# Performance work log

Measured on AMD Instinct MI355X. Metric: run time of the kernel, lower is better.

The kernel has to match this reference:

```python
import jax, jax.numpy as jnp
import numpy as np

B, N, FD = 2, 50000, 13
E = 250000
M, H = 128, 128          # message_dim, hidden_dim
EDGE_IN = 2 * FD + 8     # 34
NODE_IN = FD + 2 * M     # 269


def _mlp(x, w1, b1, w2, b2):
    return jnp.tanh(x @ w1 + b1) @ w2 + b2


def setup_inputs() -> dict:
    root = jax.random.key(0)
    k = lambda i: jax.random.fold_in(root, i)

    def lin(i, din, dout):
        w = jax.random.normal(k(i), (din, dout), jnp.float32) * np.float32(1.0 / np.sqrt(din))
        b = jax.random.normal(k(i + 100), (dout,), jnp.float32) * np.float32(0.01)
        return w, b

    ew1, eb1 = lin(1, EDGE_IN, H); ew2, eb2 = lin(2, H, M)      # mlp_edge
    ww1, wb1 = lin(3, EDGE_IN, H); ww2, wb2 = lin(4, H, 1)      # mlp_weight
    xw1, xb1 = lin(5, EDGE_IN, H); xw2, xb2 = lin(6, H, M)      # mlp_edge_world
    yw1, yb1 = lin(7, EDGE_IN, H); yw2, yb2 = lin(8, H, 1)      # mlp_weight_world
    nw1, nb1 = lin(9, NODE_IN, H); nw2, nb2 = lin(10, H, FD)    # mlp_node

    z_h = jax.random.normal(k(20), (B, N, FD), jnp.float32)
    edge_hh = jax.random.randint(k(21), (B, 2, E), 0, N, jnp.int32)
    edge_world = jax.random.randint(k(22), (B, 2, E), 0, N, jnp.int32)
    return dict(z_h=z_h, edge_hh=edge_hh, edge_world=edge_world,
                ew1=ew1, eb1=eb1, ew2=ew2, eb2=eb2,
                ww1=ww1, wb1=wb1, ww2=ww2, wb2=wb2,
                xw1=xw1, xb1=xb1, xw2=xw2, xb2=xb2,
                yw1=yw1, yb1=yb1, yw2=yw2, yb2=yb2,
                nw1=nw1, nb1=nb1, nw2=nw2, nb2=nb2)


def _edge_features(z, s, t):
    # z: (N, FD); s, t: (E,)
    pos, vel = z[:, 0:3], z[:, 3:6]
    diff = pos[s] - pos[t]                               # (E, 3)
    dist = jnp.sum(diff * diff, axis=-1, keepdims=True)  # (E, 1) squared distance
    vxc = jnp.cross(vel[s], vel[t])                      # (E, 3)
    vxn = jnp.linalg.norm(vxc, axis=-1, keepdims=True)   # (E, 1)
    return jnp.concatenate([diff, dist, vxc, vxn], axis=-1)  # (E, 8)


def reference(z_h, edge_hh, edge_world,
              ew1, eb1, ew2, eb2, ww1, wb1, ww2, wb2,
              xw1, xb1, xw2, xb2, yw1, yb1, yw2, yb2,
              nw1, nb1, nw2, nb2):
    n_nodes = z_h.shape[1]

    def per_batch(z, e_hh, e_w):
        # normal edges
        s, t = e_hh[0], e_hh[1]
        inp = jnp.concatenate([z[s], z[t], _edge_features(z, s, t)], axis=-1)  # (E, 34)
        m = _mlp(inp, ew1, eb1, ew2, eb2)                                       # (E, M)
        w = jax.nn.sigmoid(_mlp(inp, ww1, wb1, ww2, wb2))                       # (E, 1)
        agg_h = jnp.zeros((n_nodes, M), z.dtype).at[t].add(w * m)
        # world edges
        sw, tw = e_w[0], e_w[1]
        inpw = jnp.concatenate([z[sw], z[tw], _edge_features(z, sw, tw)], axis=-1)
        mw = _mlp(inpw, xw1, xb1, xw2, xb2)
        ww_ = jax.nn.sigmoid(_mlp(inpw, yw1, yb1, yw2, yb2))
        agg_w = jnp.zeros((n_nodes, M), z.dtype).at[tw].add(ww_ * mw)
        return agg_h, agg_w

    m_agg_h, m_agg_w = jax.vmap(per_batch)(z_h, edge_hh, edge_world)  # (B, N, M) each
    input_node = jnp.concatenate([z_h, m_agg_h, m_agg_w], axis=-1)    # (B, N, 269)
    delta_z_h = _mlp(input_node, nw1, nb1, nw2, nb2)                  # (B, N, 13)
    return delta_z_h
```

## Files before the change

kernel.cpp:

```cpp
#include <hip/hip_runtime.h>
#include <hip/hip_bf16.h>

#define B_   2
#define N_   50000
#define FD_  13
#define E_   250000
#define M_   128
#define H_   128

typedef __attribute__((ext_vector_type(8))) short  short8;
typedef __attribute__((ext_vector_type(8))) __bf16 bf16x8;
typedef __attribute__((ext_vector_type(4))) float  f32x4;
typedef __attribute__((ext_vector_type(8))) unsigned short ushort8;

#define MSG_BYTES  (4ull * E_ * 128 * 2)
#define HIST_BYTES (4ull * N_ * 4)
#define SORT_BYTES (4ull * E_ * 4)
#define OFF_EW1 0u
#define OFF_WW1 8192u
#define OFF_EW2 16384u
#define OFF_XW1 32768u
#define OFF_YW1 40960u
#define OFF_XW2 49152u
#define OFF_NW1 65536u
#define OFF_NW2 102400u

__device__ __forceinline__ float bf2f(unsigned short u) {
    unsigned int v = ((unsigned int)u) << 16;
    return __builtin_bit_cast(float, v);
}
__device__ __forceinline__ unsigned short f2bf(float f) {
    __bf16 h = (__bf16)f;
    return __builtin_bit_cast(unsigned short, h);
}
__device__ __forceinline__ float tanh_fast(float x) {
    float e = __expf(x + x);
    float r = __builtin_amdgcn_rcpf(e + 1.0f);
    return __builtin_fmaf(-2.0f, r, 1.0f);
}
__device__ __forceinline__ float sigmoid_fast(float x) {
    return __builtin_amdgcn_rcpf(1.0f + __expf(-x));
}
__device__ __forceinline__ f32x4 mfma16(short8 a, short8 b, f32x4 c) {
    return __builtin_amdgcn_mfma_f32_16x16x32_bf16(
        __builtin_bit_cast(bf16x8, a), __builtin_bit_cast(bf16x8, b), c, 0, 0, 0);
}

__global__ void prep_kernel(const float* __restrict__ ew1, const float* __restrict__ ww1,
                            const float* __restrict__ ew2, const float* __restrict__ xw1,
                            const float* __restrict__ yw1, const float* __restrict__ xw2,
                            const float* __restrict__ nw1, const float* __restrict__ nw2,
                            unsigned short* __restrict__ fb) {
    int m = blockIdx.y, f = blockIdx.x, l = threadIdx.x;
    const float* src; int K, Nn, KS; unsigned int off;
    switch (m) {
        case 0: src = ew1; K = 34;  Nn = 128; KS = 2; off = OFF_EW1; break;
        case 1: src = ww1; K = 34;  Nn = 128; KS = 2; off = OFF_WW1; break;
        case 2: src = ew2; K = 128; Nn = 128; KS = 4; off = OFF_EW2; break;
        case 3: src = xw1; K = 34;  Nn = 128; KS = 2; off = OFF_XW1; break;
        case 4: src = yw1; K = 34;  Nn = 128; KS = 2; off = OFF_YW1; break;
        case 5: src = xw2; K = 128; Nn = 128; KS = 4; off = OFF_XW2; break;
        case 6: src = nw1; K = 269; Nn = 128; KS = 9; off = OFF_NW1; break;
        default: src = nw2; K = 128; Nn = 13; KS = 4; off = OFF_NW2; break;
    }
    int NT = (Nn + 15) / 16;
    if (f >= KS * NT) return;
    int ks = f / NT, nt = f % NT;
    int n = nt * 16 + (l & 15);
    unsigned short* dst = fb + off + ((unsigned int)f * 64u + (unsigned int)l) * 8u;
    #pragma unroll
    for (int j = 0; j < 8; j++) {
        int k = ks * 32 + ((l >> 4) * 8) + j;
        int kk = k; bool valid = (k < K) && (n < Nn);
        if (m == 6) {
            if (k < 256)      kk = k + 13;
            else if (k < 269) kk = k - 256;
            else              valid = false;
            valid = valid && (n < Nn);
        }
        dst[j] = valid ? f2bf(src[kk * Nn + n]) : (unsigned short)0;
    }
}

__global__ void hist_kernel(const int* __restrict__ ehh, const int* __restrict__ eww,
                            int* __restrict__ hist) {
    int p = blockIdx.y, idx = blockIdx.x * 256 + threadIdx.x;
    if (idx >= E_) return;
    const int* eg = ((p >> 1) ? eww : ehh) + (size_t)(p & 1) * 2 * E_;
    atomicAdd(&hist[p * N_ + eg[E_ + idx]], 1);
}

__global__ void scan_kernel(int* __restrict__ hist) {
    __shared__ int part[1024];
    const int p = blockIdx.x, tid = threadIdx.x;
    int* h = hist + p * N_;
    const int lo = tid * 52;
    int cnt = N_ - lo; if (cnt < 0) cnt = 0; if (cnt > 52) cnt = 52;
    int v[52];
    int sum = 0;
    if (cnt == 52) {
        const int4* src = (const int4*)(h + lo);
        #pragma unroll
        for (int i = 0; i < 13; i++) {
            int4 t = src[i];
            v[4*i] = t.x; v[4*i+1] = t.y; v[4*i+2] = t.z; v[4*i+3] = t.w;
        }
        #pragma unroll
        for (int i = 0; i < 52; i++) sum += v[i];
    } else {
        for (int i = 0; i < cnt; i++) sum += h[lo + i];
    }
    part[tid] = sum;
    __syncthreads();
    for (int off = 1; off < 1024; off <<= 1) {
        int t = (tid >= off) ? part[tid - off] : 0;
        __syncthreads();
        part[tid] += t;
        __syncthreads();
    }
    int excl = (tid == 0) ? 0 : part[tid - 1];
    if (cnt == 52) {
        int4* dst = (int4*)(h + lo);
        #pragma unroll
        for (int i = 0; i < 13; i++) {
            int4 o;
            o.x = excl; excl += v[4*i];
            o.y = excl; excl += v[4*i+1];
            o.z = excl; excl += v[4*i+2];
            o.w = excl; excl += v[4*i+3];
            dst[i] = o;
        }
    } else {
        for (int i = 0; i < cnt; i++) { int t = h[lo + i]; h[lo + i] = excl; excl += t; }
    }
}

__global__ void scatter_kernel(const int* __restrict__ ehh, const int* __restrict__ eww,
                               int* __restrict__ hist, int* __restrict__ sorted) {
    int p = blockIdx.y, idx = blockIdx.x * 256 + threadIdx.x;
    if (idx >= E_) return;
    const int* eg = ((p >> 1) ? eww : ehh) + (size_t)(p & 1) * 2 * E_;
    int t = eg[E_ + idx];
    int pos = atomicAdd(&hist[p * N_ + t], 1);
    sorted[p * E_ + pos] = idx;
}

__launch_bounds__(256, 3)
__global__ void edge_kernel_msg(const float* __restrict__ z,
                                const int* __restrict__ ehh, const int* __restrict__ eww,
                                const int* __restrict__ sorted,
                                const unsigned short* __restrict__ fb,
                                unsigned short* __restrict__ msg,
                                const float* __restrict__ eb1, const float* __restrict__ wb1,
                                const float* __restrict__ ww2, const float* __restrict__ wb2,
                                const float* __restrict__ eb2,
                                const float* __restrict__ xb1, const float* __restrict__ yb1,
                                const float* __restrict__ yw2, const float* __restrict__ yb2,
                                const float* __restrict__ xb2) {
    __shared__ alignas(16) unsigned short Abuf[128][72];
    __shared__ alignas(16) unsigned short Hbuf[128][136];
    __shared__ float w_acc[128];

    const int tid  = threadIdx.x;
    const int lane = tid & 63, wv = tid >> 6, quad = lane >> 4, c = lane & 15;
    const int pass = blockIdx.y, b = pass & 1, set = pass >> 1;
    const int ebase = blockIdx.x * 128;

    const int* eg = (set ? eww : ehh) + (size_t)b * 2 * E_;
    const float* zb = z + (size_t)b * N_ * FD_;
    unsigned short* msgp = msg + (size_t)pass * E_ * 128;

    const short8* Fm1 = (const short8*)(fb + (set ? OFF_XW1 : OFF_EW1));
    const short8* Fw1 = (const short8*)(fb + (set ? OFF_YW1 : OFF_WW1));
    const short8* Fm2 = (const short8*)(fb + (set ? OFF_XW2 : OFF_EW2));
    const float* B1m = set ? xb1 : eb1;
    const float* B1w = set ? yb1 : wb1;
    const float* B2m = set ? xb2 : eb2;
    const float* Wv2 = set ? yw2 : ww2;
    const float wbias = (set ? yb2 : wb2)[0];

    const int nt0 = wv * 2;
    short8 bm[2][2], bw[2][2], b2f[2][4];
    float bias1m[2], bias1w[2], bias2m[2], w2v[2];
    #pragma unroll
    for (int i = 0; i < 2; i++) {
        int nt = nt0 + i, n = nt * 16 + c;
        #pragma unroll
        for (int ks = 0; ks < 2; ks++) { bm[i][ks] = Fm1[(ks * 8 + nt) * 64 + lane];
                                         bw[i][ks] = Fw1[(ks * 8 + nt) * 64 + lane]; }
        #pragma unroll
        for (int ks = 0; ks < 4; ks++) { b2f[i][ks] = Fm2[(ks * 8 + nt) * 64 + lane]; }
        bias1m[i] = B1m[n]; bias1w[i] = B1w[n];
        bias2m[i] = B2m[n]; w2v[i] = Wv2[n];
    }

    if (tid < 128) {
        const int e = tid;
        int sp = ebase + e; if (sp >= E_) sp = E_ - 1;
        int idx = sorted[(size_t)pass * E_ + sp];
        int s = eg[idx], t = eg[E_ + idx];
        w_acc[e] = 0.0f;
        const float* zs = zb + (size_t)s * 13;
        const float* zt = zb + (size_t)t * 13;
        float fs[13], ft[13];
        __builtin_memcpy(fs, zs, 13 * sizeof(float));
        __builtin_memcpy(ft, zt, 13 * sizeof(float));
        float d0 = fs[0] - ft[0], d1 = fs[1] - ft[1], d2 = fs[2] - ft[2];
        float dist = d0 * d0 + d1 * d1 + d2 * d2;
        float c0 = fs[4] * ft[5] - fs[5] * ft[4];
        float c1 = fs[5] * ft[3] - fs[3] * ft[5];
        float c2 = fs[3] * ft[4] - fs[4] * ft[3];
        float vxn = sqrtf(c0 * c0 + c1 * c1 + c2 * c2);
        unsigned short row[64];
        #pragma unroll
        for (int j = 0; j < 13; j++) { row[j] = f2bf(fs[j]); row[13 + j] = f2bf(ft[j]); }
        row[26] = f2bf(d0); row[27] = f2bf(d1); row[28] = f2bf(d2); row[29] = f2bf(dist);
        row[30] = f2bf(c0); row[31] = f2bf(c1); row[32] = f2bf(c2); row[33] = f2bf(vxn);
        #pragma unroll
        for (int j = 34; j < 64; j++) row[j] = 0;
        #pragma unroll
        for (int v = 0; v < 8; v++) {
            short8 sv;
            #pragma unroll
            for (int j = 0; j < 8; j++) sv[j] = (short)row[v * 8 + j];
            *((short8*)&Abuf[e][v * 8]) = sv;
        }
    }
    __syncthreads();

    #pragma unroll 1
    for (int rt = 0; rt < 8; rt++) {
        const unsigned short* ar = &Abuf[rt * 16 + c][0];
        short8 a0 = *((const short8*)(ar + quad * 8));
        short8 a1 = *((const short8*)(ar + 32 + quad * 8));
        float wpart[4] = {0.f, 0.f, 0.f, 0.f};
        #pragma unroll
        for (int i = 0; i < 2; i++) {
            f32x4 accm = {bias1m[i], bias1m[i], bias1m[i], bias1m[i]};
            f32x4 accw = {bias1w[i], bias1w[i], bias1w[i], bias1w[i]};
            accm = mfma16(a0, bm[i][0], accm);
            accm = mfma16(a1, bm[i][1], accm);
            accw = mfma16(a0, bw[i][0], accw);
            accw = mfma16(a1, bw[i][1], accw);
            int n = (nt0 + i) * 16 + c;
            #pragma unroll
            for (int r = 0; r < 4; r++) {
                Hbuf[rt * 16 + quad * 4 + r][n] = f2bf(tanh_fast(accm[r]));
                wpart[r] += tanh_fast(accw[r]) * w2v[i];
            }
        }
        #pragma unroll
        for (int r = 0; r < 4; r++) {
            float v = wpart[r];
            v += __shfl_xor(v, 1); v += __shfl_xor(v, 2);
            v += __shfl_xor(v, 4); v += __shfl_xor(v, 8);
            if (c == r) atomicAdd(&w_acc[rt * 16 + quad * 4 + r], v);
        }
    }
    __syncthreads();
    if (tid < 128) w_acc[tid] = sigmoid_fast(w_acc[tid] + wbias);
    __syncthreads();

    #pragma unroll 1
    for (int rt = 0; rt < 8; rt++) {
        const unsigned short* hr = &Hbuf[rt * 16 + c][0];
        short8 h0 = *((const short8*)(hr + quad * 8));
        short8 h1 = *((const short8*)(hr + 32 + quad * 8));
        short8 h2 = *((const short8*)(hr + 64 + quad * 8));
        short8 h3 = *((const short8*)(hr + 96 + quad * 8));
        const int elq = rt * 16 + quad * 4;
        const float g0 = w_acc[elq + 0], g1 = w_acc[elq + 1];
        const float g2 = w_acc[elq + 2], g3 = w_acc[elq + 3];
        #pragma unroll
        for (int i = 0; i < 2; i++) {
            f32x4 acc = {bias2m[i], bias2m[i], bias2m[i], bias2m[i]};
            acc = mfma16(h0, b2f[i][0], acc);
            acc = mfma16(h1, b2f[i][1], acc);
            acc = mfma16(h2, b2f[i][2], acc);
            acc = mfma16(h3, b2f[i][3], acc);
            const int n = (nt0 + i) * 16 + c;
            const float gv[4] = {g0, g1, g2, g3};
            #pragma unroll
            for (int r = 0; r < 4; r++) {
                int e = elq + r;
                if (ebase + e < E_)
                    msgp[(size_t)(ebase + e) * 128 + n] = f2bf(acc[r] * gv[r]);
            }
        }
    }
}

__launch_bounds__(256, 4)
__global__ void node_fused(const float* __restrict__ z,
                           const unsigned short* __restrict__ msg,
                           const int* __restrict__ hist,
                           const unsigned short* __restrict__ fb,
                           const float* __restrict__ nb1,
                           const float* __restrict__ nb2,
                           float* __restrict__ out) {
    __shared__ alignas(16) unsigned short Abuf[16][296];
    __shared__ alignas(16) unsigned short Hbuf[16][136];

    const int tid  = threadIdx.x;
    const int lane = tid & 63, wv = tid >> 6, quad = lane >> 4, c = lane & 15;
    const int g0 = blockIdx.x * 16;

    {
        const int nl = tid >> 4;
        const int part = tid & 15;
        const int g = g0 + nl;
        const int b = (g >= N_) ? 1 : 0;
        const int t = g - b * N_;
        #pragma unroll
        for (int s = 0; s < 2; s++) {
            const int p = s * 2 + b;
            const int end   = hist[p * N_ + t];
            const int start = (t > 0) ? hist[p * N_ + t - 1] : 0;
            float acc[8];
            #pragma unroll
            for (int k = 0; k < 8; k++) acc[k] = 0.f;
            const unsigned short* mp = msg + (size_t)p * E_ * 128 + part * 8;
            int j = start;
            for (; j + 4 <= end; j += 4) {
                ushort8 m0 = *(const ushort8*)(mp + (size_t)(j + 0) * 128);
                ushort8 m1 = *(const ushort8*)(mp + (size_t)(j + 1) * 128);
                ushort8 m2 = *(const ushort8*)(mp + (size_t)(j + 2) * 128);
                ushort8 m3 = *(const ushort8*)(mp + (size_t)(j + 3) * 128);
                #pragma unroll
                for (int k = 0; k < 8; k++)
                    acc[k] += (bf2f(m0[k]) + bf2f(m1[k])) + (bf2f(m2[k]) + bf2f(m3[k]));
            }
            for (; j < end; j++) {
                ushort8 m = *(const ushort8*)(mp + (size_t)j * 128);
                #pragma unroll
                for (int k = 0; k < 8; k++) acc[k] += bf2f(m[k]);
            }
            ushort8 u;
            #pragma unroll
            for (int k = 0; k < 8; k++) u[k] = f2bf(acc[k]);
            *((ushort8*)&Abuf[nl][s * 128 + part * 8]) = u;
        }
    }
    for (int j = tid; j < 16 * 13; j += 256) {
        int nl = j / 13, k = j % 13;
        Abuf[nl][256 + k] = f2bf(z[(size_t)(g0 + nl) * 13 + k]);
    }
    for (int j = tid; j < 16 * 19; j += 256) {
        int nl = j / 19, k = j % 19;
        Abuf[nl][269 + k] = 0;
    }
    __syncthreads();

    {
        const short8* F1 = (const short8*)(fb + OFF_NW1);
        const int nt0 = wv * 2;
        const float b1a = nb1[nt0 * 16 + c];
        const float b1b = nb1[(nt0 + 1) * 16 + c];
        f32x4 acc0 = {b1a, b1a, b1a, b1a};
        f32x4 acc1 = {b1b, b1b, b1b, b1b};
        #pragma unroll
        for (int ks = 0; ks < 9; ks++) {
            short8 a = *((const short8*)(&Abuf[c][0] + ks * 32 + quad * 8));
            acc0 = mfma16(a, F1[(ks * 8 + nt0) * 64 + lane], acc0);
            acc1 = mfma16(a, F1[(ks * 8 + nt0 + 1) * 64 + lane], acc1);
        }
        #pragma unroll
        for (int r = 0; r < 4; r++) {
            Hbuf[quad * 4 + r][nt0 * 16 + c]       = f2bf(tanh_fast(acc0[r]));
            Hbuf[quad * 4 + r][(nt0 + 1) * 16 + c] = f2bf(tanh_fast(acc1[r]));
        }
    }
    __syncthreads();

    if (wv == 0) {
        const short8* F2 = (const short8*)(fb + OFF_NW2);
        const float bias2 = (c < 13) ? nb2[c] : 0.0f;
        f32x4 acc = {bias2, bias2, bias2, bias2};
        #pragma unroll
        for (int ks = 0; ks < 4; ks++) {
            short8 h = *((const short8*)(&Hbuf[c][0] + ks * 32 + quad * 8));
            acc = mfma16(h, F2[ks * 64 + lane], acc);
        }
        #pragma unroll
        for (int r = 0; r < 4; r++) {
            int g = g0 + quad * 4 + r;
            if (c < 13) out[(size_t)g * 13 + c] = acc[r];
        }
    }
}

extern "C" void kernel_launch(void* const* d_in, const int* in_sizes, int n_in,
                              void* d_out, int out_size, void* d_ws, size_t ws_size,
                              hipStream_t stream) {
    const float* z   = (const float*)d_in[0];
    const int* ehh   = (const int*)d_in[1];
    const int* eww   = (const int*)d_in[2];
    const float* ew1 = (const float*)d_in[3];
    const float* eb1 = (const float*)d_in[4];
    const float* ew2 = (const float*)d_in[5];
    const float* eb2 = (const float*)d_in[6];
    const float* ww1 = (const float*)d_in[7];
    const float* wb1 = (const float*)d_in[8];
    const float* ww2 = (const float*)d_in[9];
    const float* wb2 = (const float*)d_in[10];
    const float* xw1 = (const float*)d_in[11];
    const float* xb1 = (const float*)d_in[12];
    const float* xw2 = (const float*)d_in[13];
    const float* xb2 = (const float*)d_in[14];
    const float* yw1 = (const float*)d_in[15];
    const float* yb1 = (const float*)d_in[16];
    const float* yw2 = (const float*)d_in[17];
    const float* yb2 = (const float*)d_in[18];
    const float* nw1 = (const float*)d_in[19];
    const float* nb1 = (const float*)d_in[20];
    const float* nw2 = (const float*)d_in[21];
    const float* nb2 = (const float*)d_in[22];

    unsigned short* msg = (unsigned short*)d_ws;
    int* hist   = (int*)((char*)d_ws + MSG_BYTES);
    int* sorted = (int*)((char*)d_ws + MSG_BYTES + HIST_BYTES);
    unsigned short* frag = (unsigned short*)((char*)d_ws + MSG_BYTES + HIST_BYTES + SORT_BYTES);

    hipMemsetAsync(hist, 0, HIST_BYTES, stream);
    prep_kernel<<<dim3(72, 8), 64, 0, stream>>>(ew1, ww1, ew2, xw1, yw1, xw2, nw1, nw2, frag);
    hist_kernel<<<dim3((E_ + 255) / 256, 4), 256, 0, stream>>>(ehh, eww, hist);
    scan_kernel<<<4, 1024, 0, stream>>>(hist);
    scatter_kernel<<<dim3((E_ + 255) / 256, 4), 256, 0, stream>>>(ehh, eww, hist, sorted);
    edge_kernel_msg<<<dim3((E_ + 127) / 128, 4), 256, 0, stream>>>(
        z, ehh, eww, sorted, frag, msg,
        eb1, wb1, ww2, wb2, eb2,
        xb1, yb1, yw2, yb2, xb2);
    node_fused<<<(B_ * N_) / 16, 256, 0, stream>>>(
        z, msg, hist, frag, nb1, nb2, (float*)d_out);
}
```

Measured before the change: 449.2 us.

## Shrink edge kernel LDS, swap MFMA operands for packed message stores, raise occupancy

The edge kernel's shared buffers shrink. The A tile drops to 48 columns, keeping only the real 34 input features plus padding, and the hidden buffer holds 64 rows processed in two rounds. This allows four blocks per CU instead of three. The second GEMM swaps its A and B operands so each lane owns four consecutive output columns of one edge, turning scattered 2-byte stores into packed 8-byte stores, and the sigmoid gate moves into that loop. The node kernel's launch bound rises to 6, which risks register spills, and the extra barriers per round add synchronisation cost.

```diff
diff --git a/kernel.cpp b/kernel.cpp
--- a/kernel.cpp
+++ b/kernel.cpp
@@ -145,7 +145,7 @@
     sorted[p * E_ + pos] = idx;
 }
 
-__launch_bounds__(256, 3)
+__launch_bounds__(256, 4)
 __global__ void edge_kernel_msg(const float* __restrict__ z,
                                 const int* __restrict__ ehh, const int* __restrict__ eww,
                                 const int* __restrict__ sorted,
@@ -157,8 +157,8 @@
                                 const float* __restrict__ xb1, const float* __restrict__ yb1,
                                 const float* __restrict__ yw2, const float* __restrict__ yb2,
                                 const float* __restrict__ xb2) {
-    __shared__ alignas(16) unsigned short Abuf[128][72];
-    __shared__ alignas(16) unsigned short Hbuf[128][136];
+    __shared__ alignas(16) unsigned short Abuf[128][48];
+    __shared__ alignas(16) unsigned short Hbuf[64][136];
     __shared__ float w_acc[128];
 
     const int tid  = threadIdx.x;
@@ -179,19 +179,22 @@
     const float* Wv2 = set ? yw2 : ww2;
     const float wbias = (set ? yb2 : wb2)[0];
 
-    const int nt0 = wv * 2;
+    const int mt0 = wv * 2;
     short8 bm[2][2], bw[2][2], b2f[2][4];
-    float bias1m[2], bias1w[2], bias2m[2], w2v[2];
+    float bias1m[2], bias1w[2], w2v[2];
+    float bias2v[2][4];
     #pragma unroll
     for (int i = 0; i < 2; i++) {
-        int nt = nt0 + i, n = nt * 16 + c;
+        int nt = mt0 + i, n = nt * 16 + c;
         #pragma unroll
         for (int ks = 0; ks < 2; ks++) { bm[i][ks] = Fm1[(ks * 8 + nt) * 64 + lane];
                                          bw[i][ks] = Fw1[(ks * 8 + nt) * 64 + lane]; }
         #pragma unroll
         for (int ks = 0; ks < 4; ks++) { b2f[i][ks] = Fm2[(ks * 8 + nt) * 64 + lane]; }
         bias1m[i] = B1m[n]; bias1w[i] = B1w[n];
-        bias2m[i] = B2m[n]; w2v[i] = Wv2[n];
+        w2v[i] = Wv2[n];
+        #pragma unroll
+        for (int r = 0; r < 4; r++) bias2v[i][r] = B2m[nt * 16 + quad * 4 + r];
     }
 
     if (tid < 128) {
@@ -211,15 +214,15 @@
         float c1 = fs[5] * ft[3] - fs[3] * ft[5];
         float c2 = fs[3] * ft[4] - fs[4] * ft[3];
         float vxn = sqrtf(c0 * c0 + c1 * c1 + c2 * c2);
-        unsigned short row[64];
+        unsigned short row[40];
         #pragma unroll
         for (int j = 0; j < 13; j++) { row[j] = f2bf(fs[j]); row[13 + j] = f2bf(ft[j]); }
         row[26] = f2bf(d0); row[27] = f2bf(d1); row[28] = f2bf(d2); row[29] = f2bf(dist);
         row[30] = f2bf(c0); row[31] = f2bf(c1); row[32] = f2bf(c2); row[33] = f2bf(vxn);
         #pragma unroll
-        for (int j = 34; j < 64; j++) row[j] = 0;
-        #pragma unroll
-        for (int v = 0; v < 8; v++) {
+        for (int j = 34; j < 40; j++) row[j] = 0;
+        #pragma unroll
+        for (int v = 0; v < 5; v++) {
             short8 sv;
             #pragma unroll
             for (int j = 0; j < 8; j++) sv[j] = (short)row[v * 8 + j];
@@ -229,68 +232,72 @@
     __syncthreads();
 
     #pragma unroll 1
-    for (int rt = 0; rt < 8; rt++) {
-        const unsigned short* ar = &Abuf[rt * 16 + c][0];
-        short8 a0 = *((const short8*)(ar + quad * 8));
-        short8 a1 = *((const short8*)(ar + 32 + quad * 8));
-        float wpart[4] = {0.f, 0.f, 0.f, 0.f};
-        #pragma unroll
-        for (int i = 0; i < 2; i++) {
-            f32x4 accm = {bias1m[i], bias1m[i], bias1m[i], bias1m[i]};
-            f32x4 accw = {bias1w[i], bias1w[i], bias1w[i], bias1w[i]};
-            accm = mfma16(a0, bm[i][0], accm);
-            accm = mfma16(a1, bm[i][1], accm);
-            accw = mfma16(a0, bw[i][0], accw);
-            accw = mfma16(a1, bw[i][1], accw);
-            int n = (nt0 + i) * 16 + c;
+    for (int round = 0; round < 2; round++) {
+        #pragma unroll 1
+        for (int rt4 = 0; rt4 < 4; rt4++) {
+            const int rt = round * 4 + rt4;
+            const unsigned short* ar = &Abuf[rt * 16 + c][0];
+            short8 a0 = *((const short8*)(ar + quad * 8));
+            short8 a1 = {};
+            if (quad == 0) a1 = *((const short8*)(ar + 32));
+            float wpart[4] = {0.f, 0.f, 0.f, 0.f};
+            #pragma unroll
+            for (int i = 0; i < 2; i++) {
+                f32x4 accm = {bias1m[i], bias1m[i], bias1m[i], bias1m[i]};
+                f32x4 accw = {bias1w[i], bias1w[i], bias1w[i], bias1w[i]};
+                accm = mfma16(a0, bm[i][0], accm);
+                accm = mfma16(a1, bm[i][1], accm);
+                accw = mfma16(a0, bw[i][0], accw);
+                accw = mfma16(a1, bw[i][1], accw);
+                int n = (mt0 + i) * 16 + c;
+                #pragma unroll
+                for (int r = 0; r < 4; r++) {
+                    Hbuf[rt4 * 16 + quad * 4 + r][n] = f2bf(tanh_fast(accm[r]));
+                    wpart[r] += tanh_fast(accw[r]) * w2v[i];
+                }
+            }
             #pragma unroll
             for (int r = 0; r < 4; r++) {
-                Hbuf[rt * 16 + quad * 4 + r][n] = f2bf(tanh_fast(accm[r]));
-                wpart[r] += tanh_fast(accw[r]) * w2v[i];
+                float v = wpart[r];
+                v += __shfl_xor(v, 1); v += __shfl_xor(v, 2);
+                v += __shfl_xor(v, 4); v += __shfl_xor(v, 8);
+                if (c == r) atomicAdd(&w_acc[rt * 16 + quad * 4 + r], v);
             }
         }
-        #pragma unroll
-        for (int r = 0; r < 4; r++) {
-            float v = wpart[r];
-            v += __shfl_xor(v, 1); v += __shfl_xor(v, 2);
-            v += __shfl_xor(v, 4); v += __shfl_xor(v, 8);
-            if (c == r) atomicAdd(&w_acc[rt * 16 + quad * 4 + r], v);
-        }
-    }
-    __syncthreads();
-    if (tid < 128) w_acc[tid] = sigmoid_fast(w_acc[tid] + wbias);
-    __syncthreads();
-
-    #pragma unroll 1
-    for (int rt = 0; rt < 8; rt++) {
-        const unsigned short* hr = &Hbuf[rt * 16 + c][0];
-        short8 h0 = *((const short8*)(hr + quad * 8));
-        short8 h1 = *((const short8*)(hr + 32 + quad * 8));
-        short8 h2 = *((const short8*)(hr + 64 + quad * 8));
-        short8 h3 = *((const short8*)(hr + 96 + quad * 8));
-        const int elq = rt * 16 + quad * 4;
-        const float g0 = w_acc[elq + 0], g1 = w_acc[elq + 1];
-        const float g2 = w_acc[elq + 2], g3 = w_acc[elq + 3];
-        #pragma unroll
-        for (int i = 0; i < 2; i++) {
-            f32x4 acc = {bias2m[i], bias2m[i], bias2m[i], bias2m[i]};
-            acc = mfma16(h0, b2f[i][0], acc);
-            acc = mfma16(h1, b2f[i][1], acc);
-            acc = mfma16(h2, b2f[i][2], acc);
-            acc = mfma16(h3, b2f[i][3], acc);
-            const int n = (nt0 + i) * 16 + c;
-            const float gv[4] = {g0, g1, g2, g3};
-            #pragma unroll
-            for (int r = 0; r < 4; r++) {
-                int e = elq + r;
-                if (ebase + e < E_)
-                    msgp[(size_t)(ebase + e) * 128 + n] = f2bf(acc[r] * gv[r]);
+        __syncthreads();
+
+        #pragma unroll 1
+        for (int nt4 = 0; nt4 < 4; nt4++) {
+            const int nt = round * 4 + nt4;
+            const int e_in = nt * 16 + c;
+            const unsigned short* hr = &Hbuf[nt4 * 16 + c][0];
+            short8 h0 = *((const short8*)(hr + quad * 8));
+            short8 h1 = *((const short8*)(hr + 32 + quad * 8));
+            short8 h2 = *((const short8*)(hr + 64 + quad * 8));
+            short8 h3 = *((const short8*)(hr + 96 + quad * 8));
+            const float g = sigmoid_fast(w_acc[e_in] + wbias);
+            const bool valid = (ebase + e_in) < E_;
+            #pragma unroll
+            for (int i = 0; i < 2; i++) {
+                f32x4 acc = {bias2v[i][0], bias2v[i][1], bias2v[i][2], bias2v[i][3]};
+                acc = mfma16(b2f[i][0], h0, acc);
+                acc = mfma16(b2f[i][1], h1, acc);
+                acc = mfma16(b2f[i][2], h2, acc);
+                acc = mfma16(b2f[i][3], h3, acc);
+                if (valid) {
+                    unsigned int lo = ((unsigned int)f2bf(acc[1]) << 16) | (unsigned int)f2bf(acc[0] * g) | ((unsigned int)f2bf(acc[1] * g) << 16);
+                    lo = (unsigned int)f2bf(acc[0] * g) | ((unsigned int)f2bf(acc[1] * g) << 16);
+                    unsigned int hi = (unsigned int)f2bf(acc[2] * g) | ((unsigned int)f2bf(acc[3] * g) << 16);
+                    uint2 pk; pk.x = lo; pk.y = hi;
+                    *(uint2*)(msgp + (size_t)(ebase + e_in) * 128 + (mt0 + i) * 16 + quad * 4) = pk;
+                }
             }
         }
-    }
-}
-
-__launch_bounds__(256, 4)
+        __syncthreads();
+    }
+}
+
+__launch_bounds__(256, 6)
 __global__ void node_fused(const float* __restrict__ z,
                            const unsigned short* __restrict__ msg,
                            const int* __restrict__ hist,
@@ -341,8 +348,8 @@
             *((ushort8*)&Abuf[nl][s * 128 + part * 8]) = u;
         }
     }
-    for (int j = tid; j < 16 * 13; j += 256) {
-        int nl = j / 13, k = j % 13;
+    if (tid < 16 * 13) {
+        int nl = tid / 13, k = tid % 13;
         Abuf[nl][256 + k] = f2bf(z[(size_t)(g0 + nl) * 13 + k]);
     }
     for (int j = tid; j < 16 * 19; j += 256) {
```

Measured after the change: 473.9 us. 5.5% more time.
